# Kernel tuning notes

Measured on AMD Instinct MI355X. Metric: run time of the kernel, lower is better.

The kernel has to match this reference:

```python
import jax, jax.numpy as jnp
import numpy as np

B, S, C, H = 2, 2048, 1280, 20
D = C // H  # head_dim = 64


def setup_inputs() -> dict:
    key = jax.random.key(0)
    ks = jax.random.split(key, 5)
    scale = 1.0 / np.sqrt(C)
    return {
        "hidden_states": jax.random.normal(ks[0], (B, S, C), dtype=jnp.float32),
        "Wq": jax.random.normal(ks[1], (C, C), dtype=jnp.float32) * scale,
        "Wk": jax.random.normal(ks[2], (C, C), dtype=jnp.float32) * scale,
        "Wv": jax.random.normal(ks[3], (C, C), dtype=jnp.float32) * scale,
        "Wo": jax.random.normal(ks[4], (C, C), dtype=jnp.float32) * scale,
        "bo": jnp.zeros((C,), dtype=jnp.float32),
    }


def reference(hidden_states, Wq, Wk, Wv, Wo, bo):
    residual = hidden_states
    # q/k/v projections (self-attention: encoder_hidden_states is None)
    q = hidden_states @ Wq  # [B,S,C]
    k = hidden_states @ Wk
    v = hidden_states @ Wv
    # split heads -> [B,H,S,D]
    q = q.reshape(B, S, H, D).transpose(0, 2, 1, 3)
    k = k.reshape(B, S, H, D).transpose(0, 2, 1, 3)
    v = v.reshape(B, S, H, D).transpose(0, 2, 1, 3)
    scale = 1.0 / np.sqrt(D)
    scores = jnp.einsum('bhqd,bhkd->bhqk', q, k) * scale  # [B,H,S,S]
    attn_probs = jax.nn.softmax(scores, axis=-1)
    # loss term: Frobenius norm of the full attention-prob tensor (fp32)
    loss = jnp.sqrt(jnp.sum(jnp.square(attn_probs.astype(jnp.float32))))
    out = jnp.einsum('bhqk,bhkd->bhqd', attn_probs, v)  # [B,H,S,D]
    out = out.transpose(0, 2, 1, 3).reshape(B, S, C)
    out = out @ Wo + bo
    out = out + residual  # residual_connection=True, rescale_output_factor=1.0
    return out, loss
```

## Files before the change

### kernel.cpp

```cpp
#include <hip/hip_runtime.h>
#include <hip/hip_bf16.h>
#include <math.h>

#define B_SZ   2
#define S_LEN  2048
#define C_DIM  1280
#define H_NUM  20
#define D_HEAD 64
#define M_TOT  (B_SZ * S_LEN)

typedef __bf16 bf16;
typedef __bf16 bf16x8 __attribute__((ext_vector_type(8)));
typedef __bf16 bf16x4 __attribute__((ext_vector_type(4)));
typedef float  f32x4  __attribute__((ext_vector_type(4)));

__device__ inline f32x4 zero4() { f32x4 z; z[0]=z[1]=z[2]=z[3]=0.f; return z; }

__device__ __forceinline__ void async_copy16(void* lds, const void* g) {
    __builtin_amdgcn_global_load_lds(
        (const __attribute__((address_space(1))) unsigned int*)g,
        (__attribute__((address_space(3))) unsigned int*)lds,
        16, 0, 0);
}

__global__ __launch_bounds__(256) void k_convert_hs(const float* __restrict__ in,
                                                    bf16* __restrict__ out) {
    int i = (blockIdx.x * 256 + threadIdx.x) * 4;
    float4 v = *(const float4*)(in + i);
    bf16x4 o; o[0]=(bf16)v.x; o[1]=(bf16)v.y; o[2]=(bf16)v.z; o[3]=(bf16)v.w;
    *(bf16x4*)(out + i) = o;
}

__global__ __launch_bounds__(256) void k_transpose_w(
    const float* __restrict__ w0, const float* __restrict__ w1,
    const float* __restrict__ w2, const float* __restrict__ w3,
    bf16* __restrict__ o0, bf16* __restrict__ o1,
    bf16* __restrict__ o2, bf16* __restrict__ o3) {
    __shared__ float t[32][33];
    const float* w = blockIdx.z==0 ? w0 : blockIdx.z==1 ? w1 : blockIdx.z==2 ? w2 : w3;
    bf16*       o  = blockIdx.z==0 ? o0 : blockIdx.z==1 ? o1 : blockIdx.z==2 ? o2 : o3;
    int k0 = blockIdx.y*32, n0 = blockIdx.x*32;
    int tx = threadIdx.x & 31, ty = threadIdx.x >> 5;
    #pragma unroll
    for (int i = 0; i < 32; i += 8)
        t[ty+i][tx] = w[(size_t)(k0+ty+i)*C_DIM + n0 + tx];
    __syncthreads();
    #pragma unroll
    for (int i = 0; i < 32; i += 8)
        o[(size_t)(n0+ty+i)*C_DIM + k0 + tx] = (bf16)t[tx][ty+i];
}

#define BM 128
#define BN 128
#define BK 64

#define GEMM_STAGE(Al, Bl, Aptr, Bptr, m0, n0, k0)                                \
    {                                                                             \
        _Pragma("unroll")                                                         \
        for (int c = 0; c < 4; ++c) {                                             \
            int p = c*256 + tid;                                                  \
            int row = p >> 3, gp = p & 7, gc = gp ^ (row & 7);                    \
            async_copy16((char*)Al + p*16,                                        \
                         &Aptr[(size_t)((m0)+row)*C_DIM + (k0) + gc*8]);          \
            async_copy16((char*)Bl + p*16,                                        \
                         &Bptr[(size_t)((n0)+row)*C_DIM + (k0) + gc*8]);          \
        }                                                                         \
    }

#define GEMM_COMPUTE(Al, Bl)                                                      \
    {                                                                             \
        _Pragma("unroll")                                                         \
        for (int kk = 0; kk < 2; ++kk) {                                          \
            bf16x8 af[4], bfr[4];                                                 \
            _Pragma("unroll")                                                     \
            for (int mf = 0; mf < 4; ++mf) {                                      \
                int arow = wm*64 + mf*16 + lr;                                    \
                af[mf] = *(const bf16x8*)((char*)Al + arow*128 +                  \
                          (((kk*4 + g) ^ (arow & 7)) << 4));                      \
            }                                                                     \
            _Pragma("unroll")                                                     \
            for (int nf = 0; nf < 4; ++nf) {                                      \
                int brow = wn*64 + nf*16 + lr;                                    \
                bfr[nf] = *(const bf16x8*)((char*)Bl + brow*128 +                 \
                          (((kk*4 + g) ^ (brow & 7)) << 4));                      \
            }                                                                     \
            _Pragma("unroll")                                                     \
            for (int mf = 0; mf < 4; ++mf)                                        \
                _Pragma("unroll")                                                 \
                for (int nf = 0; nf < 4; ++nf)                                    \
                    acc[mf][nf] = __builtin_amdgcn_mfma_f32_16x16x32_bf16(        \
                        af[mf], bfr[nf], acc[mf][nf], 0,0,0);                     \
        }                                                                         \
    }

__global__ __launch_bounds__(256) void k_gemm_qkv(
    const bf16* __restrict__ A,
    const bf16* __restrict__ WqT, const bf16* __restrict__ WkT, const bf16* __restrict__ WvT,
    bf16* __restrict__ Qo, bf16* __restrict__ Ko, bf16* __restrict__ VTo) {
    __shared__ bf16 Al[BM][BK];
    __shared__ bf16 Bl[BN][BK];
    const int z = blockIdx.z;
    const bf16* BT = z==0 ? WqT : z==1 ? WkT : WvT;
    const float scale = (z==0) ? 0.18033688011112042f : 1.0f;
    const int m0 = blockIdx.y * BM, n0 = blockIdx.x * BN;
    const int tid = threadIdx.x, lane = tid & 63, wid = tid >> 6;
    const int wm = wid >> 1, wn = wid & 1;
    const int g = lane >> 4, lr = lane & 15;
    f32x4 acc[4][4];
    #pragma unroll
    for (int i=0;i<4;i++)
        #pragma unroll
        for (int j=0;j<4;j++)
            acc[i][j] = zero4();
    for (int k0 = 0; k0 < C_DIM; k0 += BK) {
        GEMM_STAGE(Al, Bl, A, BT, m0, n0, k0);
        __syncthreads();
        GEMM_COMPUTE(Al, Bl);
        __syncthreads();
    }
    if (z == 2) {
        #pragma unroll
        for (int mf=0;mf<4;mf++) {
            #pragma unroll
            for (int nf=0;nf<4;nf++) {
                int n = n0 + wn*64 + nf*16 + lr;
                int h = n >> 6, d = n & 63;
                int m = m0 + wm*64 + mf*16 + g*4;
                int b = m >> 11, s = m & (S_LEN-1);
                bf16x4 ov;
                #pragma unroll
                for (int r=0;r<4;r++) ov[r] = (bf16)acc[mf][nf][r];
                *(bf16x4*)&VTo[((size_t)(b*H_NUM + h)*D_HEAD + d)*S_LEN + s] = ov;
            }
        }
    } else {
        bf16* Out = (z==0) ? Qo : Ko;
        #pragma unroll
        for (int mf=0;mf<4;mf++) {
            #pragma unroll
            for (int nf=0;nf<4;nf++) {
                int n = n0 + wn*64 + nf*16 + lr;
                int h = n >> 6, d = n & 63;
                #pragma unroll
                for (int r=0;r<4;r++) {
                    int m = m0 + wm*64 + mf*16 + g*4 + r;
                    int b = m >> 11, s = m & (S_LEN-1);
                    Out[(size_t)((b*H_NUM + h)*S_LEN + s)*D_HEAD + d] = (bf16)(acc[mf][nf][r] * scale);
                }
            }
        }
    }
}

__global__ __launch_bounds__(256) void k_gemm_out(
    const bf16* __restrict__ A,
    const bf16* __restrict__ WoT,
    const float* __restrict__ bo,
    const float* __restrict__ res,
    float* __restrict__ out) {
    __shared__ bf16 Al[BM][BK];
    __shared__ bf16 Bl[BN][BK];
    const int m0 = blockIdx.y * BM, n0 = blockIdx.x * BN;
    const int tid = threadIdx.x, lane = tid & 63, wid = tid >> 6;
    const int wm = wid >> 1, wn = wid & 1;
    const int g = lane >> 4, lr = lane & 15;
    f32x4 acc[4][4];
    #pragma unroll
    for (int i=0;i<4;i++)
        #pragma unroll
        for (int j=0;j<4;j++)
            acc[i][j] = zero4();
    for (int k0 = 0; k0 < C_DIM; k0 += BK) {
        GEMM_STAGE(Al, Bl, A, WoT, m0, n0, k0);
        __syncthreads();
        GEMM_COMPUTE(Al, Bl);
        __syncthreads();
    }
    #pragma unroll
    for (int mf=0;mf<4;mf++) {
        #pragma unroll
        for (int nf=0;nf<4;nf++) {
            int n = n0 + wn*64 + nf*16 + lr;
            float bias = bo[n];
            #pragma unroll
            for (int r=0;r<4;r++) {
                int m = m0 + wm*64 + mf*16 + g*4 + r;
                size_t idx = (size_t)m*C_DIM + n;
                out[idx] = acc[mf][nf][r] + bias + res[idx];
            }
        }
    }
}

#define KVB 64
__global__ __launch_bounds__(256) void k_attn(
    const bf16* __restrict__ Q,
    const bf16* __restrict__ Kg,
    const bf16* __restrict__ VT,
    bf16* __restrict__ O,
    float* __restrict__ lossPart) {
    __shared__ bf16 Kl[2][KVB][64];
    __shared__ bf16 Vl[2][D_HEAD][64];

    const int id  = blockIdx.x;
    const int fid = (id & 7) * 160 + (id >> 3);
    const int bh = fid >> 5;
    const int qb = fid & 31;
    const int b = bh / H_NUM, hh = bh % H_NUM;
    const int tid = threadIdx.x, lane = tid & 63, wid = tid >> 6;
    const int g = lane >> 4, lr = lane & 15;

    const bf16* Kbase = Kg + (size_t)bh * S_LEN * D_HEAD;
    const bf16* Vbase = VT + (size_t)bh * D_HEAD * S_LEN;

    const int qrow = qb*64 + wid*16 + lr;
    const bf16* qp = Q + ((size_t)bh*S_LEN + qrow)*D_HEAD;
    const bf16x8 aq0 = *(const bf16x8*)(qp + g*8);
    const bf16x8 aq1 = *(const bf16x8*)(qp + 32 + g*8);

    bf16x8 ones;
    #pragma unroll
    for (int i=0;i<8;i++) ones[i] = (bf16)1.0f;

    const int lb7 = (lr & 3) | (((lr >> 2) & 1) << 2);
    const int lhi = ((lr >> 2) & 2) << 3;

    f32x4 o_acc[4];
    #pragma unroll
    for (int i=0;i<4;i++) o_acc[i] = zero4();
    f32x4 l_acc = zero4();
    f32x4 s2m   = zero4();

#define STAGE(buf, kv0)                                                          \
    {                                                                            \
        _Pragma("unroll")                                                        \
        for (int pp=0; pp<2; ++pp) {                                             \
            int p = pp*256 + tid;                                                \
            int lrow = p >> 3, gp = p & 7;                                       \
            int tl = (lrow & 51) | ((lrow & 4) << 1) | ((lrow & 8) >> 1);        \
            async_copy16((char*)&Kl[buf][0][0] + p*16,                           \
                         Kbase + (size_t)((kv0) + tl)*D_HEAD                     \
                               + ((gp ^ (lrow & 7)) << 3));                      \
        }                                                                        \
        _Pragma("unroll")                                                        \
        for (int pp=0; pp<2; ++pp) {                                             \
            int p = pp*256 + tid;                                                \
            int drow = p >> 3, gp = p & 7;                                       \
            async_copy16((char*)&Vl[buf][0][0] + p*16,                           \
                         Vbase + (size_t)drow*S_LEN + (kv0)                      \
                               + ((gp ^ (drow & 7)) << 3));                      \
        }                                                                        \
    }

    STAGE(0, 0);
    __syncthreads();

    for (int t = 0; t < S_LEN/KVB; ++t) {
        const int cur = t & 1;
        if (t + 1 < S_LEN/KVB) STAGE(cur^1, (t+1)*KVB);
        const bf16* KB = &Kl[cur][0][0];
        const bf16* VB = &Vl[cur][0][0];

        f32x4 accp[2][2];
        __builtin_amdgcn_s_setprio(1);
        #pragma unroll
        for (int pair=0; pair<2; ++pair)
            #pragma unroll
            for (int u=0; u<2; ++u) {
                const bf16* kr = KB + (pair*32 + (u<<3) + lhi + lb7)*64;
                bf16x8 k0 = *(const bf16x8*)(kr + ((g       ^ lb7) << 3));
                bf16x8 k1 = *(const bf16x8*)(kr + (((4 + g) ^ lb7) << 3));
                f32x4 c = zero4();
                c = __builtin_amdgcn_mfma_f32_16x16x32_bf16(k0, aq0, c, 0,0,0);
                c = __builtin_amdgcn_mfma_f32_16x16x32_bf16(k1, aq1, c, 0,0,0);
                accp[pair][u] = c;
            }
        __builtin_amdgcn_s_setprio(0);
        bf16x8 pb[2];
        #pragma unroll
        for (int pair=0; pair<2; ++pair)
            #pragma unroll
            for (int u=0; u<2; ++u)
                #pragma unroll
                for (int r=0; r<4; ++r) {
                    float e = __builtin_amdgcn_exp2f(accp[pair][u][r]);
                    pb[pair][u*4+r] = (bf16)e;
                }
        __builtin_amdgcn_s_setprio(1);
        l_acc = __builtin_amdgcn_mfma_f32_16x16x32_bf16(ones, pb[0], l_acc, 0,0,0);
        l_acc = __builtin_amdgcn_mfma_f32_16x16x32_bf16(ones, pb[1], l_acc, 0,0,0);
        s2m = __builtin_amdgcn_mfma_f32_16x16x32_bf16(pb[0], pb[0], s2m, 0,0,0);
        s2m = __builtin_amdgcn_mfma_f32_16x16x32_bf16(pb[1], pb[1], s2m, 0,0,0);
        #pragma unroll
        for (int ds_=0; ds_<4; ++ds_) {
            const bf16* vr = VB + (ds_*16 + lr)*64;
            #pragma unroll
            for (int pair=0; pair<2; ++pair) {
                bf16x8 v = *(const bf16x8*)(vr + (((pair*4 + g) ^ (lr & 7)) << 3));
                o_acc[ds_] = __builtin_amdgcn_mfma_f32_16x16x32_bf16(v, pb[pair], o_acc[ds_], 0,0,0);
            }
        }
        __builtin_amdgcn_s_setprio(0);
        __syncthreads();
    }

    const float lfull = l_acc[0];

    const float inv = 1.0f / lfull;
    bf16* orow = O + ((size_t)(b*S_LEN + qrow)*H_NUM + hh)*D_HEAD;
    #pragma unroll
    for (int ds_=0; ds_<4; ++ds_) {
        bf16x4 ov;
        #pragma unroll
        for (int r=0; r<4; ++r) ov[r] = (bf16)(o_acc[ds_][r] * inv);
        *(bf16x4*)(orow + ds_*16 + g*4) = ov;
    }
    float v = 0.f;
    if (g == (lr >> 2)) v = s2m[lr & 3] / (lfull * lfull);
    #pragma unroll
    for (int msk=1; msk<64; msk<<=1) v += __shfl_xor(v, msk);
    if (lane == 0) lossPart[(bh*32 + qb)*4 + wid] = v;
}

__global__ __launch_bounds__(256) void k_loss(const float* __restrict__ part,
                                              float* __restrict__ out, int n) {
    __shared__ float w[4];
    float s = 0.f;
    for (int i = threadIdx.x; i < n; i += 256) s += part[i];
    #pragma unroll
    for (int msk=1; msk<64; msk<<=1) s += __shfl_xor(s, msk);
    int lane = threadIdx.x & 63, wid = threadIdx.x >> 6;
    if (lane==0) w[wid] = s;
    __syncthreads();
    if (threadIdx.x==0) out[(size_t)M_TOT*C_DIM] = sqrtf(w[0]+w[1]+w[2]+w[3]);
}

extern "C" void kernel_launch(void* const* d_in, const int* in_sizes, int n_in,
                              void* d_out, int out_size, void* d_ws, size_t ws_size,
                              hipStream_t stream) {
    (void)in_sizes; (void)n_in; (void)out_size; (void)ws_size;
    const float* hs = (const float*)d_in[0];
    const float* Wq = (const float*)d_in[1];
    const float* Wk = (const float*)d_in[2];
    const float* Wv = (const float*)d_in[3];
    const float* Wo = (const float*)d_in[4];
    const float* bo = (const float*)d_in[5];
    float* out = (float*)d_out;

    constexpr size_t HS_E = (size_t)M_TOT * C_DIM;
    constexpr size_t W_E  = (size_t)C_DIM * C_DIM;
    char* ws = (char*)d_ws;
    size_t off = 0;
    bf16* hs_bf = (bf16*)(ws + off); off += HS_E * 2;
    bf16* WqT   = (bf16*)(ws + off); off += W_E * 2;
    bf16* WkT   = (bf16*)(ws + off); off += W_E * 2;
    bf16* WvT   = (bf16*)(ws + off); off += W_E * 2;
    bf16* WoT   = (bf16*)(ws + off); off += W_E * 2;
    bf16* Qb    = (bf16*)(ws + off); off += HS_E * 2;
    bf16* Kb    = (bf16*)(ws + off); off += HS_E * 2;
    bf16* Vtb   = (bf16*)(ws + off); off += HS_E * 2;
    bf16* Ob    = (bf16*)(ws + off); off += HS_E * 2;
    float* lossPart = (float*)(ws + off); off += 5120 * 4;

    k_convert_hs<<<HS_E/(256*4), 256, 0, stream>>>(hs, hs_bf);
    k_transpose_w<<<dim3(C_DIM/32, C_DIM/32, 4), 256, 0, stream>>>(Wq, Wk, Wv, Wo, WqT, WkT, WvT, WoT);
    k_gemm_qkv<<<dim3(C_DIM/BN, M_TOT/BM, 3), 256, 0, stream>>>(hs_bf, WqT, WkT, WvT, Qb, Kb, Vtb);
    k_attn<<<1280, 256, 0, stream>>>(Qb, Kb, Vtb, Ob, lossPart);
    k_gemm_out<<<dim3(C_DIM/BN, M_TOT/BM), 256, 0, stream>>>(Ob, WoT, bo, hs, out);
    k_loss<<<1, 256, 0, stream>>>(lossPart, out, 5120);
}
```

Measured before the change: 187.6 us.

## Rewrite QKV GEMM with 256x256 tiles and triple-buffered async LDS pipeline

```diff
diff --git a/kernel.cpp b/kernel.cpp
--- a/kernel.cpp
+++ b/kernel.cpp
@@ -48,6 +48,110 @@
     #pragma unroll
     for (int i = 0; i < 32; i += 8)
         o[(size_t)(n0+ty+i)*C_DIM + k0 + tx] = (bf16)t[tx][ty+i];
+}
+
+#define QBM 256
+#define QBN 256
+#define QBK 32
+#define QNT (C_DIM / QBK)
+__global__ __launch_bounds__(512, 2) void k_gemm_qkv(
+    const bf16* __restrict__ A,
+    const bf16* __restrict__ Wcat,
+    bf16* __restrict__ Qo, bf16* __restrict__ Ko, bf16* __restrict__ VTo) {
+    __shared__ bf16 lds[3][2][QBM][QBK];
+    const int m0  = blockIdx.y * QBM;
+    const int nx  = blockIdx.x;
+    const int z   = nx / 5;
+    const int nw0 = (nx % 5) * QBN;
+    const int ng0 = nx * QBN;
+    const int tid = threadIdx.x, lane = tid & 63, wid = tid >> 6;
+    const int wm = wid >> 2, wn = wid & 3;
+    const int g = lane >> 4, lr = lane & 15;
+    const float scale = (z==0) ? 0.18033688011112042f : 1.0f;
+
+    f32x4 acc[8][4];
+    #pragma unroll
+    for (int i=0;i<8;i++)
+        #pragma unroll
+        for (int j=0;j<4;j++)
+            acc[i][j] = zero4();
+
+#define QSTAGE(bf, kt)                                                       \
+    { const int k0_ = (kt)*QBK;                                              \
+      _Pragma("unroll")                                                      \
+      for (int c = 0; c < 2; ++c) {                                          \
+        int p = c*512 + tid;                                                 \
+        int row = p >> 2, gp = p & 3;                                        \
+        async_copy16((char*)&lds[bf][0][0][0] + p*16,                        \
+                     &A[(size_t)(m0+row)*C_DIM + k0_ + gp*8]);               \
+        async_copy16((char*)&lds[bf][1][0][0] + p*16,                        \
+                     &Wcat[(size_t)(ng0+row)*C_DIM + k0_ + gp*8]);           \
+      } }
+
+    QSTAGE(0, 0);
+    QSTAGE(1, 1);
+    asm volatile("s_waitcnt vmcnt(4)" ::: "memory");
+    __builtin_amdgcn_s_barrier();
+
+    int cur = 0;
+    for (int t = 0; t < QNT; ++t) {
+        if (t + 2 < QNT) {
+            int sb = cur + 2; if (sb >= 3) sb -= 3;
+            QSTAGE(sb, t + 2);
+        }
+        const bf16* AB = &lds[cur][0][0][0];
+        const bf16* BB = &lds[cur][1][0][0];
+        bf16x8 af[8], bfr[4];
+        #pragma unroll
+        for (int mf = 0; mf < 8; ++mf)
+            af[mf] = *(const bf16x8*)(AB + (wm*128 + mf*16 + lr)*QBK + g*8);
+        #pragma unroll
+        for (int nf = 0; nf < 4; ++nf)
+            bfr[nf] = *(const bf16x8*)(BB + (wn*64 + nf*16 + lr)*QBK + g*8);
+        #pragma unroll
+        for (int mf = 0; mf < 8; ++mf)
+            #pragma unroll
+            for (int nf = 0; nf < 4; ++nf)
+                acc[mf][nf] = __builtin_amdgcn_mfma_f32_16x16x32_bf16(
+                    af[mf], bfr[nf], acc[mf][nf], 0,0,0);
+        if (t + 2 < QNT) asm volatile("s_waitcnt vmcnt(4) lgkmcnt(0)" ::: "memory");
+        else             asm volatile("s_waitcnt vmcnt(0) lgkmcnt(0)" ::: "memory");
+        __builtin_amdgcn_s_barrier();
+        if (++cur == 3) cur = 0;
+    }
+
+    if (z == 2) {
+        #pragma unroll
+        for (int mf=0;mf<8;mf++) {
+            #pragma unroll
+            for (int nf=0;nf<4;nf++) {
+                int n = nw0 + wn*64 + nf*16 + lr;
+                int h = n >> 6, d = n & 63;
+                int m = m0 + wm*128 + mf*16 + g*4;
+                int b = m >> 11, s = m & (S_LEN-1);
+                bf16x4 ov;
+                #pragma unroll
+                for (int r=0;r<4;r++) ov[r] = (bf16)acc[mf][nf][r];
+                *(bf16x4*)&VTo[((size_t)(b*H_NUM + h)*D_HEAD + d)*S_LEN + s] = ov;
+            }
+        }
+    } else {
+        bf16* Out = (z==0) ? Qo : Ko;
+        #pragma unroll
+        for (int mf=0;mf<8;mf++) {
+            #pragma unroll
+            for (int nf=0;nf<4;nf++) {
+                int n = nw0 + wn*64 + nf*16 + lr;
+                int h = n >> 6, d = n & 63;
+                #pragma unroll
+                for (int r=0;r<4;r++) {
+                    int m = m0 + wm*128 + mf*16 + g*4 + r;
+                    int b = m >> 11, s = m & (S_LEN-1);
+                    Out[(size_t)((b*H_NUM + h)*S_LEN + s)*D_HEAD + d] = (bf16)(acc[mf][nf][r] * scale);
+                }
+            }
+        }
+    }
 }
 
 #define BM 128
@@ -93,65 +197,6 @@
         }                                                                         \
     }
 
-__global__ __launch_bounds__(256) void k_gemm_qkv(
-    const bf16* __restrict__ A,
-    const bf16* __restrict__ WqT, const bf16* __restrict__ WkT, const bf16* __restrict__ WvT,
-    bf16* __restrict__ Qo, bf16* __restrict__ Ko, bf16* __restrict__ VTo) {
-    __shared__ bf16 Al[BM][BK];
-    __shared__ bf16 Bl[BN][BK];
-    const int z = blockIdx.z;
-    const bf16* BT = z==0 ? WqT : z==1 ? WkT : WvT;
-    const float scale = (z==0) ? 0.18033688011112042f : 1.0f;
-    const int m0 = blockIdx.y * BM, n0 = blockIdx.x * BN;
-    const int tid = threadIdx.x, lane = tid & 63, wid = tid >> 6;
-    const int wm = wid >> 1, wn = wid & 1;
-    const int g = lane >> 4, lr = lane & 15;
-    f32x4 acc[4][4];
-    #pragma unroll
-    for (int i=0;i<4;i++)
-        #pragma unroll
-        for (int j=0;j<4;j++)
-            acc[i][j] = zero4();
-    for (int k0 = 0; k0 < C_DIM; k0 += BK) {
-        GEMM_STAGE(Al, Bl, A, BT, m0, n0, k0);
-        __syncthreads();
-        GEMM_COMPUTE(Al, Bl);
-        __syncthreads();
-    }
-    if (z == 2) {
-        #pragma unroll
-        for (int mf=0;mf<4;mf++) {
-            #pragma unroll
-            for (int nf=0;nf<4;nf++) {
-                int n = n0 + wn*64 + nf*16 + lr;
-                int h = n >> 6, d = n & 63;
-                int m = m0 + wm*64 + mf*16 + g*4;
-                int b = m >> 11, s = m & (S_LEN-1);
-                bf16x4 ov;
-                #pragma unroll
-                for (int r=0;r<4;r++) ov[r] = (bf16)acc[mf][nf][r];
-                *(bf16x4*)&VTo[((size_t)(b*H_NUM + h)*D_HEAD + d)*S_LEN + s] = ov;
-            }
-        }
-    } else {
-        bf16* Out = (z==0) ? Qo : Ko;
-        #pragma unroll
-        for (int mf=0;mf<4;mf++) {
-            #pragma unroll
-            for (int nf=0;nf<4;nf++) {
-                int n = n0 + wn*64 + nf*16 + lr;
-                int h = n >> 6, d = n & 63;
-                #pragma unroll
-                for (int r=0;r<4;r++) {
-                    int m = m0 + wm*64 + mf*16 + g*4 + r;
-                    int b = m >> 11, s = m & (S_LEN-1);
-                    Out[(size_t)((b*H_NUM + h)*S_LEN + s)*D_HEAD + d] = (bf16)(acc[mf][nf][r] * scale);
-                }
-            }
-        }
-    }
-}
-
 __global__ __launch_bounds__(256) void k_gemm_out(
     const bf16* __restrict__ A,
     const bf16* __restrict__ WoT,
@@ -364,7 +409,7 @@
 
     k_convert_hs<<<HS_E/(256*4), 256, 0, stream>>>(hs, hs_bf);
     k_transpose_w<<<dim3(C_DIM/32, C_DIM/32, 4), 256, 0, stream>>>(Wq, Wk, Wv, Wo, WqT, WkT, WvT, WoT);
-    k_gemm_qkv<<<dim3(C_DIM/BN, M_TOT/BM, 3), 256, 0, stream>>>(hs_bf, WqT, WkT, WvT, Qb, Kb, Vtb);
+    k_gemm_qkv<<<dim3(3*C_DIM/QBN, M_TOT/QBM), 512, 0, stream>>>(hs_bf, WqT, Qb, Kb, Vtb);
     k_attn<<<1280, 256, 0, stream>>>(Qb, Kb, Vtb, Ob, lossPart);
     k_gemm_out<<<dim3(C_DIM/BN, M_TOT/BM), 256, 0, stream>>>(Ob, WoT, bo, hs, out);
     k_loss<<<1, 256, 0, stream>>>(lossPart, out, 5120);
```

Result: faster. 175.3 us (-6.5%).
